# Kernel tuning notes

Measured on AMD Instinct MI355X. Metric: run time of the kernel, lower is better.

## Reference

```python
import jax, jax.numpy as jnp
import numpy as np

T, B = 512, 64
D = [2048, 128]; P = [512, 128]; H = [256, 128]
A, S, OUT = 128, 128, 256
SC = 0.05


def setup_inputs() -> dict:
    key = jax.random.key(0)
    ks = iter(jax.random.split(key, 64))
    def n(shape, sc=SC):
        return jax.random.normal(next(ks), shape, dtype=jnp.float32) * sc
    inp = {
        "x0": n((T, B, D[0]), 1.0),
        "x1": n((T, B, D[1]), 1.0),
        "s": n((B, S), 1.0),
    }
    for m in range(2):
        k = str(m)
        C = 2 * H[m]
        inp["emb_w" + k] = n((D[m], P[m])); inp["emb_b" + k] = n((P[m],))
        inp["fx_w" + k] = n((P[m], 4 * H[m])); inp["fx_b" + k] = n((4 * H[m],))
        inp["fh_w" + k] = n((H[m], 4 * H[m]))
        inp["bx_w" + k] = n((P[m], 4 * H[m])); inp["bx_b" + k] = n((4 * H[m],))
        inp["bh_w" + k] = n((H[m], 4 * H[m]))
        inp["atV_w" + k] = n((C, A)); inp["atV_b" + k] = n((A,))
        inp["atW_w" + k] = n((S, A)); inp["atW_b" + k] = n((A,))
        inp["atw_w" + k] = n((A, 1)); inp["atw_b" + k] = n((1,))
        inp["lgd_w" + k] = n((C, OUT)); inp["lgd_b" + k] = n((OUT,))
    return inp


def _lstm_scan(xg, Wh, reverse=False):
    # xg: [T,B,4H] precomputed input projections; Wh: [H,4H]
    Tn, Bn, H4 = xg.shape
    Hn = H4 // 4
    def step(carry, xt):
        c, h = carry
        g = xt + h @ Wh
        a, i, f, o = jnp.split(g, 4, axis=-1)  # chunk order as in torch.split
        c = jnp.tanh(a) * jax.nn.sigmoid(i) + c * jax.nn.sigmoid(f)
        h = jnp.tanh(c) * jax.nn.sigmoid(o)
        return (c, h), h
    init = (jnp.zeros((Bn, Hn), xg.dtype), jnp.zeros((Bn, Hn), xg.dtype))
    _, hs = jax.lax.scan(step, init, xg, reverse=reverse)
    return hs  # [T,B,H]


def _encode_mod(x, emb_w, emb_b, fx_w, fx_b, fh_w, bx_w, bx_b, bh_w):
    h0 = x @ emb_w + emb_b                       # [T,B,P]
    hf = _lstm_scan(h0 @ fx_w + fx_b, fh_w)      # forward LSTM
    hb = _lstm_scan(h0 @ bx_w + bx_b, bh_w, reverse=True)  # backward LSTM
    return jnp.concatenate([hf, hb], axis=-1)    # [T,B,2H]


def _attend(h, s, atV_w, atV_b, atW_w, atW_b, atw_w, atw_b):
    vh = h @ atV_w + atV_b                       # [T,B,A]
    ws = s @ atW_w + atW_b                       # [B,A]
    logits = (jnp.tanh(vh + ws) @ atw_w)[..., 0] + atw_b[0]  # [T,B]
    a = jax.nn.softmax(logits, axis=0)           # exp / sum over time (stable)
    return (a[..., None] * h).mean(0)            # [B,2H]; original uses mean over T


def _forward(x0, x1, s,
             emb_w0, emb_b0, fx_w0, fx_b0, fh_w0, bx_w0, bx_b0, bh_w0,
             atV_w0, atV_b0, atW_w0, atW_b0, atw_w0, atw_b0, lgd_w0, lgd_b0,
             emb_w1, emb_b1, fx_w1, fx_b1, fh_w1, bx_w1, bx_b1, bh_w1,
             atV_w1, atV_b1, atW_w1, atW_b1, atw_w1, atw_b1, lgd_w1, lgd_b1):
    h0 = _encode_mod(x0, emb_w0, emb_b0, fx_w0, fx_b0, fh_w0, bx_w0, bx_b0, bh_w0)
    h1 = _encode_mod(x1, emb_w1, emb_b1, fx_w1, fx_b1, fh_w1, bx_w1, bx_b1, bh_w1)
    c0 = _attend(h0, s, atV_w0, atV_b0, atW_w0, atW_b0, atw_w0, atw_b0)
    c1 = _attend(h1, s, atV_w1, atV_b1, atW_w1, atW_b1, atw_w1, atw_b1)
    g = (c0 @ lgd_w0 + lgd_b0) + (c1 @ lgd_w1 + lgd_b1)  # simple modality fusion
    return jnp.tanh(g)  # [B,OUT]


def reference(x0, x1, s,
              emb_w0, emb_b0, fx_w0, fx_b0, fh_w0, bx_w0, bx_b0, bh_w0,
              atV_w0, atV_b0, atW_w0, atW_b0, atw_w0, atw_b0, lgd_w0, lgd_b0,
              emb_w1, emb_b1, fx_w1, fx_b1, fh_w1, bx_w1, bx_b1, bh_w1,
              atV_w1, atV_b1, atW_w1, atW_b1, atw_w1, atw_b1, lgd_w1, lgd_b1):
    return _forward(x0, x1, s,
                    emb_w0, emb_b0, fx_w0, fx_b0, fh_w0, bx_w0, bx_b0, bh_w0,
                    atV_w0, atV_b0, atW_w0, atW_b0, atw_w0, atw_b0, lgd_w0, lgd_b0,
                    emb_w1, emb_b1, fx_w1, fx_b1, fh_w1, bx_w1, bx_b1, bh_w1,
                    atV_w1, atV_b1, atW_w1, atW_b1, atw_w1, atw_b1, lgd_w1, lgd_b1)
```

## Files before the change

### kernel.cpp

```cpp
#include <hip/hip_runtime.h>

typedef __attribute__((ext_vector_type(4))) float  f32x4;
typedef __attribute__((ext_vector_type(8))) short  short8;
typedef __attribute__((ext_vector_type(4))) short  short4v;
typedef __attribute__((ext_vector_type(4))) int    int4v;

__device__ __forceinline__ float bf2f(short s){
  unsigned u = ((unsigned)(unsigned short)s) << 16;
  float f; __builtin_memcpy(&f, &u, 4); return f;
}
__device__ __forceinline__ short f2bf(float x){
  unsigned u; __builtin_memcpy(&u, &x, 4);
  u = (u + 0x7fffu + ((u >> 16) & 1u)) >> 16;
  return (short)u;
}
__device__ __forceinline__ float sigm(float x){ return 1.f / (1.f + __expf(-x)); }
__device__ __forceinline__ float ftanh(float x){ return 1.f - 2.f / (__expf(2.f * x) + 1.f); }

__device__ __forceinline__ short8 ld_b128_sc1(const short* p){
  short8 r;
  asm volatile("global_load_dwordx4 %0, %1, off sc1" : "=&v"(r) : "v"(p) : "memory");
  return r;
}
__device__ __forceinline__ int4v ld_i4_sc1(const int* p){
  int4v r;
  asm volatile("global_load_dwordx4 %0, %1, off sc1" : "=&v"(r) : "v"(p) : "memory");
  return r;
}
__device__ __forceinline__ void st_dword_sc1(int* p, int v){
  asm volatile("global_store_dword %0, %1, off sc1" :: "v"(p), "v"(v) : "memory");
}
__device__ __forceinline__ void wait_vm0(){
  asm volatile("s_waitcnt vmcnt(0)" ::: "memory");
  __builtin_amdgcn_sched_barrier(0);
}

template<int AF32, int OF32>
__global__ __launch_bounds__(256) void gemm_bias(const void* __restrict__ Av,
                                                 const float* __restrict__ B,
                                                 const float* __restrict__ bias,
                                                 void* __restrict__ Cv,
                                                 int M, int N, int K)
{
  __shared__ __align__(16) short As[128 * 40];
  __shared__ __align__(16) short Bs[128 * 40];
  int tid  = threadIdx.x;
  int col0 = blockIdx.x * 128, row0 = blockIdx.y * 128;
  int lane = tid & 63, wave = tid >> 6;
  int wm = (wave >> 1) * 64, wn = (wave & 1) * 64;

  f32x4 acc[4][4];
  for (int mi = 0; mi < 4; mi++)
    for (int ni = 0; ni < 4; ni++)
      for (int q = 0; q < 4; q++) acc[mi][ni][q] = 0.f;

  for (int kt = 0; kt < K; kt += 32) {
    __syncthreads();
    if (AF32) {
      const float* A = (const float*)Av;
      for (int i = 0; i < 4; i++) {
        int idx = tid + i * 256;
        int r = idx >> 3, c4 = (idx & 7) << 2;
        f32x4 v = *(const f32x4*)(A + (size_t)(row0 + r) * K + kt + c4);
        short4v o;
        for (int q = 0; q < 4; q++) o[q] = f2bf(v[q]);
        *(short4v*)&As[r * 40 + c4] = o;
      }
    } else {
      const short* A = (const short*)Av;
      for (int i = 0; i < 2; i++) {
        int idx = tid + i * 256;
        int r = idx >> 2, c8 = (idx & 3) << 3;
        short8 v = *(const short8*)(A + (size_t)(row0 + r) * K + kt + c8);
        *(short8*)&As[r * 40 + c8] = v;
      }
    }
    for (int i = 0; i < 4; i++) {
      int idx = tid + i * 256;
      int kr = idx >> 5, c4 = (idx & 31) << 2;
      f32x4 v = *(const f32x4*)(B + (size_t)(kt + kr) * N + col0 + c4);
      for (int e = 0; e < 4; e++) Bs[(c4 + e) * 40 + kr] = f2bf(v[e]);
    }
    __syncthreads();

    int fr = lane & 15, fo = (lane >> 4) << 3;
    short8 af[4], bfr[4];
    for (int mi = 0; mi < 4; mi++) af[mi]  = *(short8*)&As[(wm + mi * 16 + fr) * 40 + fo];
    for (int ni = 0; ni < 4; ni++) bfr[ni] = *(short8*)&Bs[(wn + ni * 16 + fr) * 40 + fo];
    for (int mi = 0; mi < 4; mi++)
      for (int ni = 0; ni < 4; ni++)
        acc[mi][ni] = __builtin_amdgcn_mfma_f32_16x16x32_bf16(af[mi], bfr[ni], acc[mi][ni], 0, 0, 0);
  }

  int efr = lane & 15, efrow = (lane >> 4) << 2;
  for (int ni = 0; ni < 4; ni++) {
    int col = col0 + wn + ni * 16 + efr;
    float bv = bias[col];
    for (int mi = 0; mi < 4; mi++) {
      for (int q = 0; q < 4; q++) {
        int row = row0 + wm + mi * 16 + efrow + q;
        float v = acc[mi][ni][q] + bv;
        if (OF32) ((float*)Cv)[(size_t)row * N + col] = v;
        else      ((short*)Cv)[(size_t)row * N + col] = f2bf(v);
      }
    }
  }
}

__global__ __launch_bounds__(128) void att_ws_kernel(const float* __restrict__ s,
                                                     const float* __restrict__ atW,
                                                     const float* __restrict__ atWb,
                                                     float* __restrict__ ws)
{
  int b = blockIdx.x, a = threadIdx.x;
  float acc = atWb[a];
  for (int k = 0; k < 128; k++) acc += s[b * 128 + k] * atW[k * 128 + a];
  ws[b * 128 + a] = acc;
}

template<int H, int NB>
__device__ __forceinline__ void persistent_scan(
    const short* __restrict__ xg, const float* __restrict__ Wh,
    short* __restrict__ hall, int* __restrict__ flags,
    int wg, int dir, float* gl)
{
  constexpr int C = 2 * H, H4 = 4 * H, KB = H / 32;
  int tid = threadIdx.x, lane = tid & 63, w = tid >> 6;
  int j0 = wg * 8, dircol = dir ? H : 0;
  int n = lane & 15, ko = (lane >> 4) << 3;

  short8 bw[2][KB];
#pragma unroll
  for (int nt = 0; nt < 2; nt++) {
    int col = (n >> 2) * H + j0 + nt * 4 + (n & 3);
#pragma unroll
    for (int kb = 0; kb < KB; kb++)
#pragma unroll
      for (int e = 0; e < 8; e++)
        bw[nt][kb][e] = f2bf(Wh[(size_t)(kb * 32 + ko + e) * H4 + col]);
  }

  int batch0 = w * 16 + ((lane >> 4) << 2);
  int rowA   = w * 16 + n;
  int eb = tid >> 2, ejp = tid & 3;
  float c0 = 0.f, c1 = 0.f;

  int t = dir ? 511 : 0;
  short xgr[2][4];
#pragma unroll
  for (int nt = 0; nt < 2; nt++) {
    int col = (n >> 2) * H + j0 + nt * 4 + (n & 3);
#pragma unroll
    for (int q = 0; q < 4; q++)
      xgr[nt][q] = xg[(size_t)(t * 64 + batch0 + q) * H4 + col];
  }

  for (int s = 0; s < 512; s++) {
    t = dir ? 511 - s : s;
    f32x4 acc[2];
#pragma unroll
    for (int q = 0; q < 4; q++) { acc[0][q] = 0.f; acc[1][q] = 0.f; }

    if (s > 0) {
      int tprev = dir ? t + 1 : t - 1;
      const short* hb = hall + ((size_t)tprev * 64 + rowA) * C + dircol;
      short8 hv[KB];
#pragma unroll
      for (int kb = 0; kb < KB; kb++)
        hv[kb] = ld_b128_sc1(hb + kb * 32 + ko);
      wait_vm0();
#pragma unroll
      for (int kb = 0; kb < KB; kb++) {
        acc[0] = __builtin_amdgcn_mfma_f32_16x16x32_bf16(hv[kb], bw[0][kb], acc[0], 0, 0, 0);
        acc[1] = __builtin_amdgcn_mfma_f32_16x16x32_bf16(hv[kb], bw[1][kb], acc[1], 0, 0, 0);
      }
    }

#pragma unroll
    for (int nt = 0; nt < 2; nt++) {
      int gcol = (n >> 2) * 8 + nt * 4 + (n & 3);
#pragma unroll
      for (int q = 0; q < 4; q++)
        gl[(batch0 + q) * 33 + gcol] = acc[nt][q] + bf2f(xgr[nt][q]);
    }
    __syncthreads();

    {
      const float* gb = gl + eb * 33 + ejp * 2;
      float a0 = gb[0],  a1 = gb[1];
      float i0 = gb[8],  i1 = gb[9];
      float f0 = gb[16], f1 = gb[17];
      float o0 = gb[24], o1 = gb[25];
      c0 = ftanh(a0) * sigm(i0) + c0 * sigm(f0);
      c1 = ftanh(a1) * sigm(i1) + c1 * sigm(f1);
      unsigned h0 = (unsigned short)f2bf(ftanh(c0) * sigm(o0));
      unsigned h1 = (unsigned short)f2bf(ftanh(c1) * sigm(o1));
      st_dword_sc1((int*)(hall + ((size_t)t * 64 + eb) * C + dircol + j0 + ejp * 2),
                   (int)(h0 | (h1 << 16)));
    }

    if (s < 511) {
      wait_vm0();
      __syncthreads();
      if (tid == 0) st_dword_sc1(flags + wg, s + 1);

      int tn = dir ? t - 1 : t + 1;
#pragma unroll
      for (int nt = 0; nt < 2; nt++) {
        int col = (n >> 2) * H + j0 + nt * 4 + (n & 3);
#pragma unroll
        for (int q = 0; q < 4; q++)
          xgr[nt][q] = xg[(size_t)(tn * 64 + batch0 + q) * H4 + col];
      }

      if (tid == 0) {
        for (;;) {
          int4v f[NB / 4];
#pragma unroll
          for (int i = 0; i < NB / 4; i++) f[i] = ld_i4_sc1(flags + i * 4);
          wait_vm0();
          int ok = 1;
#pragma unroll
          for (int i = 0; i < NB / 4; i++)
#pragma unroll
            for (int j = 0; j < 4; j++) ok &= (f[i][j] > s);
          if (ok) break;
          __builtin_amdgcn_s_sleep(1);
        }
      }
      __syncthreads();
    }
  }
}

__global__ __launch_bounds__(256) void lstm_persistent(
    const short* __restrict__ xgf0, const short* __restrict__ xgb0,
    const short* __restrict__ xgf1, const short* __restrict__ xgb1,
    const float* __restrict__ fh0, const float* __restrict__ bh0,
    const float* __restrict__ fh1, const float* __restrict__ bh1,
    short* __restrict__ hall0, short* __restrict__ hall1, int* __restrict__ bar)
{
  __shared__ float gl[64 * 33];
  int bx = blockIdx.x;
  if (bx < 64) {
    int dir = bx >> 5, wg = bx & 31;
    persistent_scan<256, 32>(dir ? xgb0 : xgf0, dir ? bh0 : fh0, hall0,
                             bar + (dir ? 64 : 0), wg, dir, gl);
  } else {
    int r = bx - 64, dir = r >> 4, wg = r & 15;
    persistent_scan<128, 16>(dir ? xgb1 : xgf1, dir ? bh1 : fh1, hall1,
                             bar + 128 + (dir ? 64 : 0), wg, dir, gl);
  }
}

__global__ __launch_bounds__(256) void logits_kernel(const float* __restrict__ vh,
                                                     const float* __restrict__ ws,
                                                     const float* __restrict__ atw,
                                                     const float* __restrict__ atwb,
                                                     float* __restrict__ lg)
{
  int wid  = (int)((blockIdx.x * 256 + threadIdx.x) >> 6);
  int lane = threadIdx.x & 63;
  if (wid >= 32768) return;
  int b = wid & 63;
  float x0 = vh[(size_t)wid * 128 + lane]      + ws[b * 128 + lane];
  float x1 = vh[(size_t)wid * 128 + 64 + lane] + ws[b * 128 + 64 + lane];
  float v = ftanh(x0) * atw[lane] + ftanh(x1) * atw[64 + lane];
  for (int off = 32; off; off >>= 1) v += __shfl_down(v, off);
  if (lane == 0) lg[wid] = v + atwb[0];
}

__global__ __launch_bounds__(256) void softmax_ctx(const float* __restrict__ lg,
                                                   const short* __restrict__ hall,
                                                   float* __restrict__ ctx, int C)
{
  int b = blockIdx.x, tid = threadIdx.x, lane = tid & 63, wv = tid >> 6;
  __shared__ float ebuf[512];
  __shared__ float red[8];
  float l0 = lg[tid * 64 + b];
  float l1 = lg[(tid + 256) * 64 + b];
  float m = fmaxf(l0, l1);
  for (int o = 32; o; o >>= 1) m = fmaxf(m, __shfl_xor(m, o));
  if (lane == 0) red[wv] = m;
  __syncthreads();
  m = fmaxf(fmaxf(red[0], red[1]), fmaxf(red[2], red[3]));
  float e0 = __expf(l0 - m), e1 = __expf(l1 - m);
  ebuf[tid] = e0; ebuf[tid + 256] = e1;
  float sm = e0 + e1;
  for (int o = 32; o; o >>= 1) sm += __shfl_xor(sm, o);
  if (lane == 0) red[4 + wv] = sm;
  __syncthreads();
  sm = red[4] + red[5] + red[6] + red[7];
  float inv = 1.f / (sm * 512.f);
  for (int c = tid; c < C; c += 256) {
    float acc = 0.f;
    const short* hp = hall + (size_t)b * C + c;
    for (int t = 0; t < 512; t++) acc += ebuf[t] * bf2f(hp[(size_t)t * 64 * C]);
    ctx[b * C + c] = acc * inv;
  }
}

__global__ __launch_bounds__(256) void final_kernel(const float* __restrict__ ctx0,
                                                    const float* __restrict__ ctx1,
                                                    const float* __restrict__ w0,
                                                    const float* __restrict__ b0,
                                                    const float* __restrict__ w1,
                                                    const float* __restrict__ b1,
                                                    float* __restrict__ out)
{
  int b = blockIdx.x, o = threadIdx.x;
  float acc = b0[o] + b1[o];
  for (int c = 0; c < 512; c++) acc += ctx0[b * 512 + c] * w0[c * 256 + o];
  for (int c = 0; c < 256; c++) acc += ctx1[b * 256 + c] * w1[c * 256 + o];
  out[b * 256 + o] = ftanh(acc);
}

extern "C" void kernel_launch(void* const* d_in, const int* in_sizes, int n_in,
                              void* d_out, int out_size, void* d_ws, size_t ws_size,
                              hipStream_t stream)
{
  const float* x0    = (const float*)d_in[0];
  const float* x1    = (const float*)d_in[1];
  const float* sIn   = (const float*)d_in[2];
  const float* emb_w0 = (const float*)d_in[3];  const float* emb_b0 = (const float*)d_in[4];
  const float* fx_w0  = (const float*)d_in[5];  const float* fx_b0  = (const float*)d_in[6];
  const float* fh_w0  = (const float*)d_in[7];
  const float* bx_w0  = (const float*)d_in[8];  const float* bx_b0  = (const float*)d_in[9];
  const float* bh_w0  = (const float*)d_in[10];
  const float* atV_w0 = (const float*)d_in[11]; const float* atV_b0 = (const float*)d_in[12];
  const float* atW_w0 = (const float*)d_in[13]; const float* atW_b0 = (const float*)d_in[14];
  const float* atw_w0 = (const float*)d_in[15]; const float* atw_b0 = (const float*)d_in[16];
  const float* lgd_w0 = (const float*)d_in[17]; const float* lgd_b0 = (const float*)d_in[18];
  const float* emb_w1 = (const float*)d_in[19]; const float* emb_b1 = (const float*)d_in[20];
  const float* fx_w1  = (const float*)d_in[21]; const float* fx_b1  = (const float*)d_in[22];
  const float* fh_w1  = (const float*)d_in[23];
  const float* bx_w1  = (const float*)d_in[24]; const float* bx_b1  = (const float*)d_in[25];
  const float* bh_w1  = (const float*)d_in[26];
  const float* atV_w1 = (const float*)d_in[27]; const float* atV_b1 = (const float*)d_in[28];
  const float* atW_w1 = (const float*)d_in[29]; const float* atW_b1 = (const float*)d_in[30];
  const float* atw_w1 = (const float*)d_in[31]; const float* atw_b1 = (const float*)d_in[32];
  const float* lgd_w1 = (const float*)d_in[33]; const float* lgd_b1 = (const float*)d_in[34];
  float* out = (float*)d_out;

  char* wp = (char*)d_ws;
  auto alloc = [&](size_t bytes) -> void* {
    void* p = wp; wp += (bytes + 255) & ~(size_t)255; return p;
  };
  int*   bar   = (int*)alloc(1024);
  short* h0_0  = (short*)alloc(32768ull * 512 * 2);
  short* h0_1  = (short*)alloc(32768ull * 128 * 2);
  short* xgf0  = (short*)alloc(32768ull * 1024 * 2);
  short* xgb0  = (short*)alloc(32768ull * 1024 * 2);
  short* xgf1  = (short*)alloc(32768ull * 512 * 2);
  short* xgb1  = (short*)alloc(32768ull * 512 * 2);
  short* hall0 = (short*)alloc(32768ull * 512 * 2);
  short* hall1 = (short*)alloc(32768ull * 256 * 2);
  float* vh0   = (float*)alloc(32768ull * 128 * 4);
  float* vh1   = (float*)alloc(32768ull * 128 * 4);
  float* wsb0  = (float*)alloc(64 * 128 * 4);
  float* wsb1  = (float*)alloc(64 * 128 * 4);
  float* lg0   = (float*)alloc(32768 * 4);
  float* lg1   = (float*)alloc(32768 * 4);
  float* ctx0  = (float*)alloc(64 * 512 * 4);
  float* ctx1  = (float*)alloc(64 * 256 * 4);

  gemm_bias<1, 0><<<dim3(4, 256), 256, 0, stream>>>(x0, emb_w0, emb_b0, h0_0, 32768, 512, 2048);
  gemm_bias<1, 0><<<dim3(1, 256), 256, 0, stream>>>(x1, emb_w1, emb_b1, h0_1, 32768, 128, 128);
  gemm_bias<0, 0><<<dim3(8, 256), 256, 0, stream>>>(h0_0, fx_w0, fx_b0, xgf0, 32768, 1024, 512);
  gemm_bias<0, 0><<<dim3(8, 256), 256, 0, stream>>>(h0_0, bx_w0, bx_b0, xgb0, 32768, 1024, 512);
  gemm_bias<0, 0><<<dim3(4, 256), 256, 0, stream>>>(h0_1, fx_w1, fx_b1, xgf1, 32768, 512, 128);
  gemm_bias<0, 0><<<dim3(4, 256), 256, 0, stream>>>(h0_1, bx_w1, bx_b1, xgb1, 32768, 512, 128);
  att_ws_kernel<<<64, 128, 0, stream>>>(sIn, atW_w0, atW_b0, wsb0);
  att_ws_kernel<<<64, 128, 0, stream>>>(sIn, atW_w1, atW_b1, wsb1);

  hipMemsetAsync(bar, 0, 1024, stream);
  lstm_persistent<<<96, 256, 0, stream>>>(xgf0, xgb0, xgf1, xgb1,
                                          fh_w0, bh_w0, fh_w1, bh_w1,
                                          hall0, hall1, bar);

  gemm_bias<0, 1><<<dim3(1, 256), 256, 0, stream>>>(hall0, atV_w0, atV_b0, vh0, 32768, 128, 512);
  gemm_bias<0, 1><<<dim3(1, 256), 256, 0, stream>>>(hall1, atV_w1, atV_b1, vh1, 32768, 128, 256);
  logits_kernel<<<8192, 256, 0, stream>>>(vh0, wsb0, atw_w0, atw_b0, lg0);
  logits_kernel<<<8192, 256, 0, stream>>>(vh1, wsb1, atw_w1, atw_b1, lg1);
  softmax_ctx<<<64, 256, 0, stream>>>(lg0, hall0, ctx0, 512);
  softmax_ctx<<<64, 256, 0, stream>>>(lg1, hall1, ctx1, 256);
  final_kernel<<<64, 256, 0, stream>>>(ctx0, ctx1, lgd_w0, lgd_b0, lgd_w1, lgd_b1, out);
}
```

Before: 2.716 ms.

## Reorder LSTM gate columns so each lane holds all four gates, dropping LDS exchange

The recurrent MFMA operands are swapped and the weight columns permuted so that each lane's accumulator holds the a/i/f/o gates for one hidden unit and batch. The cell update then runs in registers instead of going through a shared-memory gate buffer and a __syncthreads every step. Hidden outputs are gathered with shuffles and written as one 128-bit store per row rather than many dword stores. This shortens the per-step critical path of the serial 512-step scan, at the cost of extra shuffles and having only a quarter of the lanes do the stores.

```diff
diff --git a/kernel.cpp b/kernel.cpp
--- a/kernel.cpp
+++ b/kernel.cpp
@@ -26,6 +26,9 @@
   int4v r;
   asm volatile("global_load_dwordx4 %0, %1, off sc1" : "=&v"(r) : "v"(p) : "memory");
   return r;
+}
+__device__ __forceinline__ void st_b128i_sc1(short* p, int4v v){
+  asm volatile("global_store_dwordx4 %0, %1, off sc1" :: "v"(p), "v"(v) : "memory");
 }
 __device__ __forceinline__ void st_dword_sc1(int* p, int v){
   asm volatile("global_store_dword %0, %1, off sc1" :: "v"(p), "v"(v) : "memory");
@@ -122,81 +125,81 @@
 __device__ __forceinline__ void persistent_scan(
     const short* __restrict__ xg, const float* __restrict__ Wh,
     short* __restrict__ hall, int* __restrict__ flags,
-    int wg, int dir, float* gl)
+    int wg, int dir)
 {
   constexpr int C = 2 * H, H4 = 4 * H, KB = H / 32;
-  int tid = threadIdx.x, lane = tid & 63, w = tid >> 6;
-  int j0 = wg * 8, dircol = dir ? H : 0;
-  int n = lane & 15, ko = (lane >> 4) << 3;
+  const int tid = threadIdx.x, lane = tid & 63, w = tid >> 6;
+  const int j0 = wg * 8, dircol = dir ? H : 0;
+  const int n = lane & 15, rg = lane >> 4;
+  const int batch = w * 16 + n;
 
   short8 bw[2][KB];
 #pragma unroll
   for (int nt = 0; nt < 2; nt++) {
-    int col = (n >> 2) * H + j0 + nt * 4 + (n & 3);
+    int colG = (n & 3) * H + j0 + nt * 4 + (n >> 2);
 #pragma unroll
     for (int kb = 0; kb < KB; kb++)
 #pragma unroll
       for (int e = 0; e < 8; e++)
-        bw[nt][kb][e] = f2bf(Wh[(size_t)(kb * 32 + ko + e) * H4 + col]);
-  }
-
-  int batch0 = w * 16 + ((lane >> 4) << 2);
-  int rowA   = w * 16 + n;
-  int eb = tid >> 2, ejp = tid & 3;
-  float c0 = 0.f, c1 = 0.f;
-
-  int t = dir ? 511 : 0;
+        bw[nt][kb][e] = f2bf(Wh[(size_t)(kb * 32 + rg * 8 + e) * H4 + colG]);
+  }
+
+  float cst[2] = {0.f, 0.f};
+
   short xgr[2][4];
-#pragma unroll
-  for (int nt = 0; nt < 2; nt++) {
-    int col = (n >> 2) * H + j0 + nt * 4 + (n & 3);
-#pragma unroll
-    for (int q = 0; q < 4; q++)
-      xgr[nt][q] = xg[(size_t)(t * 64 + batch0 + q) * H4 + col];
+  {
+    int t0 = dir ? 511 : 0;
+#pragma unroll
+    for (int nt = 0; nt < 2; nt++)
+#pragma unroll
+      for (int g = 0; g < 4; g++)
+        xgr[nt][g] = xg[(size_t)(t0 * 64 + batch) * H4 + g * H + j0 + nt * 4 + rg];
   }
 
   for (int s = 0; s < 512; s++) {
-    t = dir ? 511 - s : s;
+    int t = dir ? 511 - s : s;
     f32x4 acc[2];
 #pragma unroll
     for (int q = 0; q < 4; q++) { acc[0][q] = 0.f; acc[1][q] = 0.f; }
 
     if (s > 0) {
       int tprev = dir ? t + 1 : t - 1;
-      const short* hb = hall + ((size_t)tprev * 64 + rowA) * C + dircol;
+      const short* hb = hall + ((size_t)tprev * 64 + batch) * C + dircol;
       short8 hv[KB];
 #pragma unroll
       for (int kb = 0; kb < KB; kb++)
-        hv[kb] = ld_b128_sc1(hb + kb * 32 + ko);
+        hv[kb] = ld_b128_sc1(hb + kb * 32 + rg * 8);
       wait_vm0();
 #pragma unroll
       for (int kb = 0; kb < KB; kb++) {
-        acc[0] = __builtin_amdgcn_mfma_f32_16x16x32_bf16(hv[kb], bw[0][kb], acc[0], 0, 0, 0);
-        acc[1] = __builtin_amdgcn_mfma_f32_16x16x32_bf16(hv[kb], bw[1][kb], acc[1], 0, 0, 0);
-      }
-    }
-
+        acc[0] = __builtin_amdgcn_mfma_f32_16x16x32_bf16(bw[0][kb], hv[kb], acc[0], 0, 0, 0);
+        acc[1] = __builtin_amdgcn_mfma_f32_16x16x32_bf16(bw[1][kb], hv[kb], acc[1], 0, 0, 0);
+      }
+    }
+
+    unsigned hpk = 0;
 #pragma unroll
     for (int nt = 0; nt < 2; nt++) {
-      int gcol = (n >> 2) * 8 + nt * 4 + (n & 3);
-#pragma unroll
-      for (int q = 0; q < 4; q++)
-        gl[(batch0 + q) * 33 + gcol] = acc[nt][q] + bf2f(xgr[nt][q]);
-    }
-    __syncthreads();
-
-    {
-      const float* gb = gl + eb * 33 + ejp * 2;
-      float a0 = gb[0],  a1 = gb[1];
-      float i0 = gb[8],  i1 = gb[9];
-      float f0 = gb[16], f1 = gb[17];
-      float o0 = gb[24], o1 = gb[25];
-      c0 = ftanh(a0) * sigm(i0) + c0 * sigm(f0);
-      c1 = ftanh(a1) * sigm(i1) + c1 * sigm(f1);
-      unsigned h0 = (unsigned short)f2bf(ftanh(c0) * sigm(o0));
-      unsigned h1 = (unsigned short)f2bf(ftanh(c1) * sigm(o1));
-      st_dword_sc1((int*)(hall + ((size_t)t * 64 + eb) * C + dircol + j0 + ejp * 2),
-                   (int)(h0 | (h1 << 16)));
+      float a_ = acc[nt][0] + bf2f(xgr[nt][0]);
+      float i_ = acc[nt][1] + bf2f(xgr[nt][1]);
+      float f_ = acc[nt][2] + bf2f(xgr[nt][2]);
+      float o_ = acc[nt][3] + bf2f(xgr[nt][3]);
+      float cc = ftanh(a_) * sigm(i_) + cst[nt] * sigm(f_);
+      cst[nt] = cc;
+      unsigned hb16 = (unsigned short)f2bf(ftanh(cc) * sigm(o_));
+      hpk |= hb16 << (16 * nt);
+    }
+    unsigned u0 = __shfl(hpk, n,      64);
+    unsigned u1 = __shfl(hpk, n + 16, 64);
+    unsigned u2 = __shfl(hpk, n + 32, 64);
+    unsigned u3 = __shfl(hpk, n + 48, 64);
+    if (rg == 0) {
+      int4v dv;
+      dv[0] = (int)((u0 & 0xffffu) | (u1 << 16));
+      dv[1] = (int)((u2 & 0xffffu) | (u3 << 16));
+      dv[2] = (int)((u0 >> 16) | (u1 & 0xffff0000u));
+      dv[3] = (int)((u2 >> 16) | (u3 & 0xffff0000u));
+      st_b128i_sc1(hall + ((size_t)t * 64 + batch) * C + dircol + j0, dv);
     }
 
     if (s < 511) {
@@ -206,12 +209,10 @@
 
       int tn = dir ? t - 1 : t + 1;
 #pragma unroll
-      for (int nt = 0; nt < 2; nt++) {
-        int col = (n >> 2) * H + j0 + nt * 4 + (n & 3);
-#pragma unroll
-        for (int q = 0; q < 4; q++)
-          xgr[nt][q] = xg[(size_t)(tn * 64 + batch0 + q) * H4 + col];
-      }
+      for (int nt = 0; nt < 2; nt++)
+#pragma unroll
+        for (int g = 0; g < 4; g++)
+          xgr[nt][g] = xg[(size_t)(tn * 64 + batch) * H4 + g * H + j0 + nt * 4 + rg];
 
       if (tid == 0) {
         for (;;) {
@@ -240,16 +241,15 @@
     const float* __restrict__ fh1, const float* __restrict__ bh1,
     short* __restrict__ hall0, short* __restrict__ hall1, int* __restrict__ bar)
 {
-  __shared__ float gl[64 * 33];
   int bx = blockIdx.x;
   if (bx < 64) {
     int dir = bx >> 5, wg = bx & 31;
     persistent_scan<256, 32>(dir ? xgb0 : xgf0, dir ? bh0 : fh0, hall0,
-                             bar + (dir ? 64 : 0), wg, dir, gl);
+                             bar + (dir ? 64 : 0), wg, dir);
   } else {
     int r = bx - 64, dir = r >> 4, wg = r & 15;
     persistent_scan<128, 16>(dir ? xgb1 : xgf1, dir ? bh1 : fh1, hall1,
-                             bar + 128 + (dir ? 64 : 0), wg, dir, gl);
+                             bar + 128 + (dir ? 64 : 0), wg, dir);
   }
 }
 
```

Result: slower. 2.826 ms (+4.0%).
